# Performance work log

Measured on AMD Instinct MI355X. Metric: run time of the kernel, lower is better.

The kernel has to match this reference:

```python
import jax, jax.numpy as jnp
import numpy as np

# Sizes: B graphs of N nodes each, K nearest neighbours, D=feat_dim=nhid, C=pos_dim
B, N, K, D, C = 4, 1024, 128, 32, 2
L = 3                     # number of EGNN conv layers
E_IN = 2 * D + 1          # edge MLP input: feats_i | feats_j | rel_dist (edge_dim=0, fourier=0)
E_H = 2 * E_IN            # edge MLP hidden


def _lin(key, fan_in, fan_out):
    kw, kb = jax.random.split(key)
    w = jax.random.normal(kw, (fan_in, fan_out), jnp.float32) / np.sqrt(fan_in)
    b = jax.random.normal(kb, (fan_out,), jnp.float32) * 0.01
    return w, b


def _stack(key, fan_in, fan_out):
    ws, bs = zip(*[_lin(k, fan_in, fan_out) for k in jax.random.split(key, L)])
    return jnp.stack(ws), jnp.stack(bs)


def setup_inputs() -> dict:
    key = jax.random.key(0)
    ks = jax.random.split(key, 10)
    feat_ = jax.random.normal(ks[0], (B * N, D), jnp.float32)
    coor_ = jax.random.normal(ks[1], (B * N, C), jnp.float32)
    batch = jnp.full((B,), N, dtype=jnp.int32)   # per-graph node counts (equal-size graphs)
    embed_w, embed_b = _lin(ks[2], D, D)         # embed: Linear(feat_dim, nhid)
    e1_w, e1_b = _stack(ks[3], E_IN, E_H)        # edge MLP
    e2_w, e2_b = _stack(ks[4], E_H, D)           # -> m_dim = nhid
    gate_w, gate_b = _stack(ks[5], D, 1)         # soft_edges gate
    c1_w, c1_b = _stack(ks[6], D, 4 * D)         # coors MLP
    c2_w, c2_b = _stack(ks[7], 4 * D, 1)
    n1_w, n1_b = _stack(ks[8], 2 * D, 2 * D)     # node MLP
    n2_w, n2_b = _stack(ks[9], 2 * D, D)
    coors_scale = jnp.full((L, 1), 1e-2, jnp.float32)  # CoorsNorm scale (init 1e-2)
    return dict(feat_=feat_, coor_=coor_, batch=batch, embed_w=embed_w, embed_b=embed_b,
                e1_w=e1_w, e1_b=e1_b, e2_w=e2_w, e2_b=e2_b, gate_w=gate_w, gate_b=gate_b,
                c1_w=c1_w, c1_b=c1_b, c2_w=c2_w, c2_b=c2_b, n1_w=n1_w, n1_b=n1_b,
                n2_w=n2_w, n2_b=n2_b, coors_scale=coors_scale)


def _lrelu(x):
    return jax.nn.leaky_relu(x, 0.1)


def _gather(x, idx):
    # x: [B, n, d], idx: [B, n, k] -> [B, n, k, d]
    return jax.vmap(lambda xb, ib: xb[ib])(x, idx)


def _egnn_layer(feats, coors, p):
    (e1_w, e1_b, e2_w, e2_b, gate_w, gate_b, c1_w, c1_b, c2_w, c2_b,
     n1_w, n1_b, n2_w, n2_b, scale) = p
    # pairwise squared distances; k smallest (self included, valid_radius=inf)
    diff = coors[:, :, None, :] - coors[:, None, :, :]      # [B,n,n,C]
    dist = jnp.sum(diff * diff, axis=-1)                    # [B,n,n]
    neg_d, idx = jax.lax.top_k(-dist, K)                    # k nearest
    rel_dist = -neg_d[..., None]                            # [B,n,K,1]
    rel_coors = coors[:, :, None, :] - _gather(coors, idx)  # [B,n,K,C]
    feats_j = _gather(feats, idx)                           # [B,n,K,D]
    feats_i = jnp.broadcast_to(feats[:, :, None, :], feats_j.shape)
    edge_in = jnp.concatenate([feats_i, feats_j, rel_dist], axis=-1)  # [B,n,K,E_IN]
    # edge MLP: Lin -> act -> Lin -> act ; soft edge gate
    m = _lrelu(_lrelu(edge_in @ e1_w + e1_b) @ e2_w + e2_b)            # [B,n,K,D]
    m = m * jax.nn.sigmoid(m @ gate_w + gate_b)
    # coordinate update: coors_mlp -> scalar weights; CoorsNorm on rel coords
    cw = (_lrelu(m @ c1_w + c1_b) @ c2_w + c2_b)[..., 0]               # [B,n,K]
    norm = jnp.maximum(jnp.linalg.norm(rel_coors, axis=-1, keepdims=True), 1e-8)
    rel_n = rel_coors / norm * scale
    coors_out = jnp.einsum('bik,bikc->bic', cw, rel_n) + coors
    # feature update: sum-pool messages, node MLP with residual
    m_i = jnp.sum(m, axis=2)                                           # [B,n,D]
    node_in = jnp.concatenate([feats, m_i], axis=-1)
    feats_out = _lrelu(node_in @ n1_w + n1_b) @ n2_w + n2_b + feats
    return feats_out, coors_out


def reference(feat_, coor_, batch, embed_w, embed_b, e1_w, e1_b, e2_w, e2_b,
              gate_w, gate_b, c1_w, c1_b, c2_w, c2_b, n1_w, n1_b, n2_w, n2_b,
              coors_scale):
    # embed MLP (dropout is identity at p=0 / eval), then batch equal-size graphs
    feats = _lrelu(feat_ @ embed_w + embed_b).reshape(B, N, D)
    coors = coor_.reshape(B, N, C)
    for l in range(L):
        p = (e1_w[l], e1_b[l], e2_w[l], e2_b[l], gate_w[l], gate_b[l],
             c1_w[l], c1_b[l], c2_w[l], c2_b[l], n1_w[l], n1_b[l],
             n2_w[l], n2_b[l], coors_scale[l])
        feats, coors = _egnn_layer(feats, coors, p)
    return feats.reshape(B * N, D)
```

## Files before the change

### kernel.cpp

```cpp
#include <hip/hip_runtime.h>
#include <hip/hip_bf16.h>
#include <math.h>

#define BB 4
#define NN 1024
#define KK 128
#define DD 32
#define LL 3
#define EH 130
#define EHP 132

typedef float f32x4 __attribute__((ext_vector_type(4)));
typedef short s16x8 __attribute__((ext_vector_type(8)));

__device__ __forceinline__ float lrelu(float x) { return fmaxf(x, 0.1f * x); }

__device__ __forceinline__ unsigned pk2(float a, float b) {
    __hip_bfloat162 h = __float22bfloat162_rn(float2{a, b});
    return *(unsigned*)&h;
}
__device__ __forceinline__ unsigned short bf16_hu(float v) {
    return (unsigned short)((__float_as_uint(v) + 0x8000u) >> 16);
}
__device__ __forceinline__ unsigned short bf16_rne(float v) {
    unsigned u = __float_as_uint(v);
    return (unsigned short)((u + 0x7fffu + ((u >> 16) & 1u)) >> 16);
}

__device__ __forceinline__ void knn_block(const float2* __restrict__ cbp, int i, int t,
                                          unsigned* __restrict__ hist,
                                          volatile unsigned* __restrict__ scr,
                                          int* __restrict__ nb) {
    const int lane = t & 63, wid = t >> 6;
    unsigned* histw = hist + wid * 256;
    const float2 ci = cbp[i];
    unsigned k[4];
#pragma unroll
    for (int s = 0; s < 4; s++) {
        float2 cj = cbp[wid * 256 + s * 64 + lane];
        float dx = ci.x - cj.x, dy = ci.y - cj.y;
        float d = __fadd_rn(__fmul_rn(dx, dx), __fmul_rn(dy, dy));
        k[s] = __float_as_uint(d);
    }
    unsigned prefix = 0u;
    unsigned r = KK - 1;
#pragma unroll
    for (int pass = 0; pass < 4; pass++) {
        const int sh = 24 - 8 * pass;
        const unsigned mpref = (pass == 0) ? 0u : (0xFFFFFFFFu << (sh + 8));
        ((uint4*)histw)[lane] = uint4{0u, 0u, 0u, 0u};
#pragma unroll
        for (int s = 0; s < 4; s++) {
            if ((k[s] & mpref) == prefix)
                atomicAdd(&histw[(k[s] >> sh) & 255u], 1u);
        }
        __syncthreads();
        unsigned tot = hist[t] + hist[256 + t] + hist[512 + t] + hist[768 + t];
        unsigned incl = tot;
#pragma unroll
        for (int off = 1; off < 64; off <<= 1) {
            unsigned v = __shfl_up(incl, off, 64);
            if (lane >= off) incl += v;
        }
        if (lane == 63) scr[wid] = incl;
        __syncthreads();
        unsigned woff = 0;
#pragma unroll
        for (int w = 0; w < 4; w++)
            if (w < wid) woff += scr[w];
        incl += woff;
        const unsigned excl = incl - tot;
        if (r >= excl && r < incl) { scr[4] = (unsigned)t; scr[5] = r - excl; }
        __syncthreads();
        prefix |= scr[4] << sh;
        r = scr[5];
    }
    const unsigned dstar = prefix;

    const unsigned long long below = (1ull << lane) - 1ull;
    unsigned long long mL[4], mE[4];
    unsigned cntL = 0, cntE = 0;
#pragma unroll
    for (int s = 0; s < 4; s++) {
        mL[s] = __ballot(k[s] < dstar);
        mE[s] = __ballot(k[s] == dstar);
        cntL += (unsigned)__popcll(mL[s]);
        cntE += (unsigned)__popcll(mE[s]);
    }
    if (lane == 0) { scr[8 + wid] = cntL; scr[12 + wid] = cntE; }
    __syncthreads();
    unsigned offL = 0, offE = 0, totalL = 0;
#pragma unroll
    for (int w = 0; w < 4; w++) {
        unsigned cl = scr[8 + w];
        if (w < wid) { offL += cl; offE += scr[12 + w]; }
        totalL += cl;
    }
    unsigned run = offL;
#pragma unroll
    for (int s = 0; s < 4; s++) {
        if (k[s] < dstar) nb[run + (unsigned)__popcll(mL[s] & below)] = wid * 256 + s * 64 + lane;
        run += (unsigned)__popcll(mL[s]);
    }
    const int need = KK - (int)totalL;
    unsigned tie = offE;
#pragma unroll
    for (int s = 0; s < 4; s++) {
        if (k[s] == dstar) {
            unsigned r2 = tie + (unsigned)__popcll(mE[s] & below);
            if ((int)r2 < need) nb[totalL + r2] = wid * 256 + s * 64 + lane;
        }
        tie += (unsigned)__popcll(mE[s]);
    }
}

__global__ __launch_bounds__(128) void prep_kernel(
    const float* __restrict__ feat,
    const float* __restrict__ ew, const float* __restrict__ eb,
    float* __restrict__ fout,
    const float* __restrict__ e1w0, const float* __restrict__ e1b0,
    float* __restrict__ HI, float* __restrict__ HJ,
    const float* __restrict__ e2w, const float* __restrict__ e2b,
    const float* __restrict__ c1w,
    unsigned short* __restrict__ e2f, unsigned short* __restrict__ c1f) {
    const int bid = blockIdx.x;
    const int t = threadIdx.x;
    if (bid < 2048) {
        __shared__ float sfe[2][DD];
        const int n0 = bid * 2;
        if (t < 64) {
            const int nl = t >> 5, o = t & 31;
            const float* f = feat + (size_t)(n0 + nl) * DD;
            float a = eb[o];
#pragma unroll
            for (int k = 0; k < DD; k++) a = fmaf(f[k], ew[k * DD + o], a);
            a = lrelu(a);
            fout[(size_t)(n0 + nl) * DD + o] = a;
            sfe[nl][o] = a;
        }
        __syncthreads();
        for (int idx = t; idx < 2 * EHP; idx += 128) {
            const int nl = idx / EHP, o = idx - nl * EHP;
            const size_t off = (size_t)(n0 + nl) * EHP + o;
            if (o >= EH) { HI[off] = 0.f; HJ[off] = 0.f; continue; }
            const float* fl = sfe[nl];
            float aa = e1b0[o], cc = 0.f;
#pragma unroll
            for (int k = 0; k < DD; k++) aa = fmaf(fl[k], e1w0[k * EH + o], aa);
#pragma unroll
            for (int k = 0; k < DD; k++) cc = fmaf(fl[k], e1w0[(DD + k) * EH + o], cc);
            HI[off] = aa;
            HJ[off] = cc;
        }
    } else {
        const int TOT_E2 = LL * 5120;
        const int TOT = TOT_E2 + LL * 4096;
        for (int u = (bid - 2048) * 128 + t; u < TOT; u += 96 * 128) {
            if (u < TOT_E2) {
                int l = u / 5120, v = u - l * 5120;
                int jj = v & 7, la = (v >> 3) & 63, nt = (v >> 9) & 1, c = v >> 10;
                int n = nt * 16 + (la & 15);
                float val;
                if (c < 4) {
                    int k = 32 * c + (la >> 4) * 8 + jj;
                    val = e2w[(size_t)l * EH * DD + k * DD + n];
                } else {
                    int ks = (la >> 4) * 8 + jj;
                    val = (ks == 0) ? e2w[((size_t)l * EH + 128) * DD + n]
                        : (ks == 1) ? e2w[((size_t)l * EH + 129) * DD + n]
                        : (ks == 2) ? e2b[(size_t)l * DD + n] : 0.f;
                }
                e2f[u] = bf16_rne(val);
            } else {
                int v = u - TOT_E2;
                int jj = v & 7, la = (v >> 3) & 63, nt = (v >> 9) & 7, l = v >> 12;
                int k = (la >> 4) * 8 + jj;
                int n = nt * 16 + (la & 15);
                c1f[v] = bf16_rne(c1w[(size_t)l * DD * 128 + k * 128 + n]);
            }
        }
    }
}

__global__ __launch_bounds__(256) void layer_kernel(
    const float* __restrict__ feats_in, const float* __restrict__ coors_in,
    const float* __restrict__ HI, const float* __restrict__ HJ,
    const float* __restrict__ w65,
    const unsigned short* __restrict__ e2f,
    const unsigned short* __restrict__ c1f,
    const float* __restrict__ gw, const float* __restrict__ gb,
    const float* __restrict__ c1b, const float* __restrict__ c2w, const float* __restrict__ c2b,
    const float* __restrict__ n1w, const float* __restrict__ n1b,
    const float* __restrict__ n2w, const float* __restrict__ n2b,
    const float* __restrict__ scale,
    const float* __restrict__ e1wn, const float* __restrict__ e1bn,
    float* __restrict__ HIn, float* __restrict__ HJn,
    float* __restrict__ feats_out, float* __restrict__ coors_out) {
    const int node = blockIdx.x;
    const int b = node >> 10;
    const int t = threadIdx.x;
    const int lane = t & 63, wid = t >> 6;
    const int ln = lane & 15, q = lane >> 4;
    const int rowbase = wid * 32;

    __shared__ __align__(16) float shi[EHP];
    __shared__ __align__(16) float sw65[EHP];
    __shared__ __align__(16) unsigned short smA[4 * 32 * 32];
    __shared__ unsigned sknn[16];
    __shared__ float sx0[128], sx1[128], su[128], sv[128], srd[128];
    __shared__ int snb[128];
    __shared__ float sgw[DD], sfi[DD], sfo[DD];
    __shared__ float sc1b[128], sc2w[128];
    __shared__ float redm[4][DD], redc[4][2];
    __shared__ float sni[2 * DD], shd[2 * DD];
    __shared__ float sp1[4][2 * DD], sp2[4][DD];

    for (int u = t; u < EHP; u += 256) {
        shi[u] = HI[(size_t)node * EHP + u];
        sw65[u] = (u < EH) ? w65[u] : 0.f;
    }
    if (t < DD) { sfi[t] = feats_in[node * DD + t]; sgw[t] = gw[t]; }
    if (t >= 128) { sc1b[t - 128] = c1b[t - 128]; sc2w[t - 128] = c2w[t - 128]; }

    knn_block((const float2*)coors_in + (size_t)b * NN, node & (NN - 1), t,
              (unsigned*)smA, sknn, snb);
    __syncthreads();

    const float cix = coors_in[node * 2], ciy = coors_in[node * 2 + 1];
    if (t < 128) {
        const int j = snb[t];
        const float2 cj = *(const float2*)(coors_in + ((size_t)(b * NN) + j) * 2);
        const float dx = cix - cj.x, dy = ciy - cj.y;
        const float rd = __fadd_rn(__fmul_rn(dx, dx), __fmul_rn(dy, dy));
        srd[t] = rd;
        const float nrm = fmaxf(sqrtf(rd), 1e-8f);
        const float s = scale[0] / nrm;
        su[t] = dx * s;
        sv[t] = dy * s;
        const float2 hjt = *(const float2*)(HJ + ((size_t)(b * NN) + j) * EHP + 128);
        sx0[t] = lrelu(shi[128] + hjt.x + rd * sw65[128]);
        sx1[t] = lrelu(shi[129] + hjt.y + rd * sw65[129]);
    }
    __syncthreads();

    float rdR[2];
    const float* hjb[2];
#pragma unroll
    for (int mt = 0; mt < 2; mt++) {
        const int row = rowbase + mt * 16 + ln;
        rdR[mt] = srd[row];
        hjb[mt] = HJ + ((size_t)(b * NN) + snb[row]) * EHP;
    }

    const float4* shi4 = (const float4*)shi;
    const float4* sw4  = (const float4*)sw65;

    const f32x4 zz = {0.f, 0.f, 0.f, 0.f};
    f32x4 accA[2][2];
    accA[0][0] = zz; accA[0][1] = zz; accA[1][0] = zz; accA[1][1] = zz;

    float4 ha[2], hbv[2];
#pragma unroll
    for (int mt = 0; mt < 2; mt++) {
        const float4* hjp = (const float4*)(hjb[mt] + q * 8);
        ha[mt] = hjp[0];
        hbv[mt] = hjp[1];
    }
    s16x8 bcur0 = *(const s16x8*)(e2f + (0 * 64 + lane) * 8);
    s16x8 bcur1 = *(const s16x8*)(e2f + (1 * 64 + lane) * 8);

#pragma unroll 1
    for (int c = 0; c < 4; c++) {
        s16x8 bn0 = *(const s16x8*)(e2f + (((c + 1) * 2 + 0) * 64 + lane) * 8);
        s16x8 bn1 = *(const s16x8*)(e2f + (((c + 1) * 2 + 1) * 64 + lane) * 8);
        float4 nha[2], nhb[2];
        if (c < 3) {
#pragma unroll
            for (int mt = 0; mt < 2; mt++) {
                const float4* hjp = (const float4*)(hjb[mt] + (c + 1) * 32 + q * 8);
                nha[mt] = hjp[0];
                nhb[mt] = hjp[1];
            }
        }
        const int kb = c * 8 + q * 2;
        const float4 hi0 = shi4[kb], hi1 = shi4[kb + 1];
        const float4 wv0 = sw4[kb],  wv1 = sw4[kb + 1];
#pragma unroll
        for (int mt = 0; mt < 2; mt++) {
            const float r = rdR[mt];
            union { s16x8 v; unsigned u[4]; } A;
            A.u[0] = pk2(lrelu(hi0.x + ha[mt].x + r * wv0.x), lrelu(hi0.y + ha[mt].y + r * wv0.y));
            A.u[1] = pk2(lrelu(hi0.z + ha[mt].z + r * wv0.z), lrelu(hi0.w + ha[mt].w + r * wv0.w));
            A.u[2] = pk2(lrelu(hi1.x + hbv[mt].x + r * wv1.x), lrelu(hi1.y + hbv[mt].y + r * wv1.y));
            A.u[3] = pk2(lrelu(hi1.z + hbv[mt].z + r * wv1.z), lrelu(hi1.w + hbv[mt].w + r * wv1.w));
            accA[mt][0] = __builtin_amdgcn_mfma_f32_16x16x32_bf16(A.v, bcur0, accA[mt][0], 0, 0, 0);
            accA[mt][1] = __builtin_amdgcn_mfma_f32_16x16x32_bf16(A.v, bcur1, accA[mt][1], 0, 0, 0);
        }
#pragma unroll
        for (int mt = 0; mt < 2; mt++) { ha[mt] = nha[mt]; hbv[mt] = nhb[mt]; }
        bcur0 = bn0; bcur1 = bn1;
    }

    {
#pragma unroll
        for (int mt = 0; mt < 2; mt++) {
            const int row = rowbase + mt * 16 + ln;
            union { s16x8 v; unsigned u[4]; } A;
            const unsigned p0 = pk2(sx0[row], sx1[row]);
            A.u[0] = (q == 0) ? p0 : 0u;
            A.u[1] = (q == 0) ? 0x00003f80u : 0u;
            A.u[2] = 0u;
            A.u[3] = 0u;
            accA[mt][0] = __builtin_amdgcn_mfma_f32_16x16x32_bf16(A.v, bcur0, accA[mt][0], 0, 0, 0);
            accA[mt][1] = __builtin_amdgcn_mfma_f32_16x16x32_bf16(A.v, bcur1, accA[mt][1], 0, 0, 0);
        }
    }

    s16x8 cfr[8];
#pragma unroll
    for (int g8 = 0; g8 < 8; g8++)
        cfr[g8] = *(const s16x8*)(c1f + (g8 * 64 + lane) * 8);

#pragma unroll
    for (int mt = 0; mt < 2; mt++)
#pragma unroll
        for (int nt = 0; nt < 2; nt++)
#pragma unroll
            for (int r = 0; r < 4; r++)
                accA[mt][nt][r] = lrelu(accA[mt][nt][r]);

    const float gbv = gb[0];
#pragma unroll
    for (int mt = 0; mt < 2; mt++) {
        float p[4];
#pragma unroll
        for (int r = 0; r < 4; r++)
            p[r] = accA[mt][0][r] * sgw[ln] + accA[mt][1][r] * sgw[16 + ln];
#pragma unroll
        for (int off = 1; off <= 8; off <<= 1)
#pragma unroll
            for (int r = 0; r < 4; r++) p[r] += __shfl_xor(p[r], off);
#pragma unroll
        for (int r = 0; r < 4; r++) {
            const float g = 1.f / (1.f + __expf(-(p[r] + gbv)));
            accA[mt][0][r] *= g;
            accA[mt][1][r] *= g;
        }
    }

    float mi0 = 0.f, mi1 = 0.f;
#pragma unroll
    for (int mt = 0; mt < 2; mt++)
#pragma unroll
        for (int r = 0; r < 4; r++) { mi0 += accA[mt][0][r]; mi1 += accA[mt][1][r]; }
    mi0 += __shfl_xor(mi0, 16); mi0 += __shfl_xor(mi0, 32);
    mi1 += __shfl_xor(mi1, 16); mi1 += __shfl_xor(mi1, 32);
    if (lane < 16) { redm[wid][lane] = mi0; redm[wid][16 + lane] = mi1; }

    unsigned short* smw = smA + wid * (32 * 32);
#pragma unroll
    for (int mt = 0; mt < 2; mt++)
#pragma unroll
        for (int nt = 0; nt < 2; nt++)
#pragma unroll
            for (int r = 0; r < 4; r++) {
                const int prow = (r << 3) | (4 * mt + q);
                smw[prow * 32 + nt * 16 + ln] = bf16_hu(accA[mt][nt][r]);
            }

    s16x8 a4[2];
#pragma unroll
    for (int mt = 0; mt < 2; mt++) {
        const int prow = ((ln & 3) << 3) | (4 * mt + (ln >> 2));
        a4[mt] = *(const s16x8*)(smw + prow * 32 + q * 8);
    }

    float cacc[2][4];
#pragma unroll
    for (int mt = 0; mt < 2; mt++)
#pragma unroll
        for (int r = 0; r < 4; r++) cacc[mt][r] = 0.f;

#pragma unroll
    for (int g = 0; g < 4; g++) {
        const float cb0 = sc1b[(2 * g + 0) * 16 + ln];
        const float cb1 = sc1b[(2 * g + 1) * 16 + ln];
        const f32x4 ci0 = {cb0, cb0, cb0, cb0};
        const f32x4 ci1 = {cb1, cb1, cb1, cb1};
        f32x4 c20[2], c21[2];
#pragma unroll
        for (int mt = 0; mt < 2; mt++) {
            c20[mt] = __builtin_amdgcn_mfma_f32_16x16x32_bf16(a4[mt], cfr[2 * g + 0], ci0, 0, 0, 0);
            c21[mt] = __builtin_amdgcn_mfma_f32_16x16x32_bf16(a4[mt], cfr[2 * g + 1], ci1, 0, 0, 0);
        }
#pragma unroll
        for (int h = 0; h < 2; h++) {
            const float c2wv = sc2w[(2 * g + h) * 16 + ln];
#pragma unroll
            for (int mt = 0; mt < 2; mt++)
#pragma unroll
                for (int r = 0; r < 4; r++) {
                    const float v = (h ? c21[mt][r] : c20[mt][r]);
                    cacc[mt][r] = fmaf(lrelu(v), c2wv, cacc[mt][r]);
                }
        }
    }
#pragma unroll
    for (int off = 1; off <= 8; off <<= 1)
#pragma unroll
        for (int mt = 0; mt < 2; mt++)
#pragma unroll
            for (int r = 0; r < 4; r++) cacc[mt][r] += __shfl_xor(cacc[mt][r], off);

    const float c2bv = c2b[0];
    float vxp = 0.f, vyp = 0.f;
    if (ln == 0) {
#pragma unroll
        for (int mt = 0; mt < 2; mt++)
#pragma unroll
            for (int r = 0; r < 4; r++) {
                const int row = rowbase + mt * 16 + q * 4 + r;
                const float cw = cacc[mt][r] + c2bv;
                vxp = fmaf(cw, su[row], vxp);
                vyp = fmaf(cw, sv[row], vyp);
            }
    }
    vxp += __shfl_xor(vxp, 16); vxp += __shfl_xor(vxp, 32);
    vyp += __shfl_xor(vyp, 16); vyp += __shfl_xor(vyp, 32);
    if (lane == 0) { redc[wid][0] = vxp; redc[wid][1] = vyp; }

    __syncthreads();
    if (t < DD) {
        sni[t] = sfi[t];
        sni[DD + t] = redm[0][t] + redm[1][t] + redm[2][t] + redm[3][t];
    }
    __syncthreads();
    {
        const int o = t & 63, p = t >> 6;
        float a = 0.f;
#pragma unroll
        for (int k = 0; k < 16; k++) a = fmaf(sni[p * 16 + k], n1w[(p * 16 + k) * 64 + o], a);
        sp1[p][o] = a;
    }
    __syncthreads();
    if (t < 2 * DD)
        shd[t] = lrelu(n1b[t] + ((sp1[0][t] + sp1[1][t]) + (sp1[2][t] + sp1[3][t])));
    __syncthreads();
    if (t < 128) {
        const int o = t & 31, p = t >> 5;
        float a = 0.f;
#pragma unroll
        for (int k = 0; k < 16; k++) a = fmaf(shd[p * 16 + k], n2w[(p * 16 + k) * DD + o], a);
        sp2[p][o] = a;
    }
    __syncthreads();
    if (t < DD) {
        const float val = n2b[t] + ((sp2[0][t] + sp2[1][t]) + (sp2[2][t] + sp2[3][t])) + sfi[t];
        feats_out[node * DD + t] = val;
        sfo[t] = val;
    }
    if (t == 0) {
        coors_out[node * 2]     = cix + redc[0][0] + redc[1][0] + redc[2][0] + redc[3][0];
        coors_out[node * 2 + 1] = ciy + redc[0][1] + redc[1][1] + redc[2][1] + redc[3][1];
    }
    __syncthreads();

    if (e1wn) {
        for (int idx = t; idx < 2 * EHP; idx += 256) {
            const int nl = idx / EHP, o = idx - nl * EHP;
            float* dst = (nl ? HJn : HIn) + (size_t)node * EHP + o;
            if (o >= EH) { *dst = 0.f; continue; }
            const int rowoff = nl ? DD : 0;
            float a = nl ? 0.f : e1bn[o];
#pragma unroll
            for (int k = 0; k < DD; k++) a = fmaf(sfo[k], e1wn[(rowoff + k) * EH + o], a);
            *dst = a;
        }
    }
}

extern "C" void kernel_launch(void* const* d_in, const int* in_sizes, int n_in,
                              void* d_out, int out_size, void* d_ws, size_t ws_size,
                              hipStream_t stream) {
    const float* feat_   = (const float*)d_in[0];
    const float* coor_   = (const float*)d_in[1];
    const float* embed_w = (const float*)d_in[3];
    const float* embed_b = (const float*)d_in[4];
    const float* e1_w    = (const float*)d_in[5];
    const float* e1_b    = (const float*)d_in[6];
    const float* e2_w    = (const float*)d_in[7];
    const float* e2_b    = (const float*)d_in[8];
    const float* gate_w  = (const float*)d_in[9];
    const float* gate_b  = (const float*)d_in[10];
    const float* c1_w    = (const float*)d_in[11];
    const float* c1_b    = (const float*)d_in[12];
    const float* c2_w    = (const float*)d_in[13];
    const float* c2_b    = (const float*)d_in[14];
    const float* n1_w    = (const float*)d_in[15];
    const float* n1_b    = (const float*)d_in[16];
    const float* n2_w    = (const float*)d_in[17];
    const float* n2_b    = (const float*)d_in[18];
    const float* cscale  = (const float*)d_in[19];

    float* ws = (float*)d_ws;
    float* fa   = ws;   ws += BB * NN * DD;
    float* fb   = ws;   ws += BB * NN * DD;
    float* ca   = ws;   ws += BB * NN * 2;
    float* cb2  = ws;   ws += BB * NN * 2;
    float* HI0  = ws;   ws += BB * NN * EHP;
    float* HJ0  = ws;   ws += BB * NN * EHP;
    float* HI1  = ws;   ws += BB * NN * EHP;
    float* HJ1  = ws;   ws += BB * NN * EHP;
    unsigned short* e2f = (unsigned short*)ws;
    unsigned short* c1f = e2f + LL * 5120;

    prep_kernel<<<2048 + 96, 128, 0, stream>>>(feat_, embed_w, embed_b, fa,
                                               e1_w, e1_b, HI0, HJ0,
                                               e2_w, e2_b, c1_w, e2f, c1f);

    float* HIbuf[2] = {HI0, HI1};
    float* HJbuf[2] = {HJ0, HJ1};
    const float* fin = fa;
    const float* cin = coor_;
    float* fouts[LL] = {fb, fa, (float*)d_out};
    float* couts[LL] = {ca, cb2, ca};

    for (int l = 0; l < LL; l++) {
        const int cur = l & 1, nxt = (l + 1) & 1;
        layer_kernel<<<BB * NN, 256, 0, stream>>>(
            fin, cin, HIbuf[cur], HJbuf[cur],
            e1_w + ((size_t)l * 65 + 64) * EH,
            e2f + (size_t)l * 5120,
            c1f + (size_t)l * 4096,
            gate_w + (size_t)l * DD,
            gate_b + l,
            c1_b + (size_t)l * 128,
            c2_w + (size_t)l * 128,
            c2_b + l,
            n1_w + (size_t)l * 64 * 64,
            n1_b + (size_t)l * 64,
            n2_w + (size_t)l * 64 * 32,
            n2_b + (size_t)l * DD,
            cscale + l,
            (l < LL - 1) ? (e1_w + (size_t)(l + 1) * 65 * EH) : nullptr,
            (l < LL - 1) ? (e1_b + (size_t)(l + 1) * EH) : nullptr,
            HIbuf[nxt], HJbuf[nxt],
            fouts[l], couts[l]);
        fin = fouts[l];
        cin = couts[l];
    }
}
```

Measured before the change: 316.8 us.

## Compute neighbor edge-MLP first layer in-kernel via split-bf16 MFMA instead of gathering HJ

Stops precomputing the per-node HI/HJ projections (130 floats each) and no longer gathers 132-float HJ rows for every neighbor. Each block now gathers the neighbor's 32-dim features, stored as bf16 hi/lo pairs, and recomputes the j-side projection with three bf16 MFMAs per tile (hi*hi, hi*lo, lo*hi) to stay near fp32 accuracy. The i-side projection is computed once per block in fp32. This cuts global gather traffic about fourfold, at the cost of extra MFMA work, LDS staging of the hidden activations, and a new prepacked weight layout.

```diff
diff --git a/kernel.cpp b/kernel.cpp
--- a/kernel.cpp
+++ b/kernel.cpp
@@ -8,7 +8,6 @@
 #define DD 32
 #define LL 3
 #define EH 130
-#define EHP 132
 
 typedef float f32x4 __attribute__((ext_vector_type(4)));
 typedef short s16x8 __attribute__((ext_vector_type(8)));
@@ -25,6 +24,9 @@
 __device__ __forceinline__ unsigned short bf16_rne(float v) {
     unsigned u = __float_as_uint(v);
     return (unsigned short)((u + 0x7fffu + ((u >> 16) & 1u)) >> 16);
+}
+__device__ __forceinline__ float bf2f(unsigned short h) {
+    return __uint_as_float(((unsigned)h) << 16);
 }
 
 __device__ __forceinline__ void knn_block(const float2* __restrict__ cbp, int i, int t,
@@ -117,16 +119,15 @@
 __global__ __launch_bounds__(128) void prep_kernel(
     const float* __restrict__ feat,
     const float* __restrict__ ew, const float* __restrict__ eb,
-    float* __restrict__ fout,
-    const float* __restrict__ e1w0, const float* __restrict__ e1b0,
-    float* __restrict__ HI, float* __restrict__ HJ,
+    float* __restrict__ fout, unsigned short* __restrict__ fouth, unsigned short* __restrict__ foutl,
+    const float* __restrict__ e1w,
     const float* __restrict__ e2w, const float* __restrict__ e2b,
     const float* __restrict__ c1w,
-    unsigned short* __restrict__ e2f, unsigned short* __restrict__ c1f) {
+    unsigned short* __restrict__ e2f, unsigned short* __restrict__ c1f,
+    unsigned short* __restrict__ e1Jh, unsigned short* __restrict__ e1Jl) {
     const int bid = blockIdx.x;
     const int t = threadIdx.x;
     if (bid < 2048) {
-        __shared__ float sfe[2][DD];
         const int n0 = bid * 2;
         if (t < 64) {
             const int nl = t >> 5, o = t & 31;
@@ -135,28 +136,19 @@
 #pragma unroll
             for (int k = 0; k < DD; k++) a = fmaf(f[k], ew[k * DD + o], a);
             a = lrelu(a);
-            fout[(size_t)(n0 + nl) * DD + o] = a;
-            sfe[nl][o] = a;
-        }
-        __syncthreads();
-        for (int idx = t; idx < 2 * EHP; idx += 128) {
-            const int nl = idx / EHP, o = idx - nl * EHP;
-            const size_t off = (size_t)(n0 + nl) * EHP + o;
-            if (o >= EH) { HI[off] = 0.f; HJ[off] = 0.f; continue; }
-            const float* fl = sfe[nl];
-            float aa = e1b0[o], cc = 0.f;
-#pragma unroll
-            for (int k = 0; k < DD; k++) aa = fmaf(fl[k], e1w0[k * EH + o], aa);
-#pragma unroll
-            for (int k = 0; k < DD; k++) cc = fmaf(fl[k], e1w0[(DD + k) * EH + o], cc);
-            HI[off] = aa;
-            HJ[off] = cc;
+            const size_t off = (size_t)(n0 + nl) * DD + o;
+            fout[off] = a;
+            const unsigned short h = bf16_rne(a);
+            fouth[off] = h;
+            foutl[off] = bf16_rne(a - bf2f(h));
         }
     } else {
-        const int TOT_E2 = LL * 5120;
-        const int TOT = TOT_E2 + LL * 4096;
-        for (int u = (bid - 2048) * 128 + t; u < TOT; u += 96 * 128) {
-            if (u < TOT_E2) {
+        const int A_ = LL * 5120;
+        const int B_ = A_ + LL * 4096;
+        const int C_ = B_ + LL * 4608;
+        const int TOT = C_ + LL * 4608;
+        for (int u = (bid - 2048) * 128 + t; u < TOT; u += 432 * 128) {
+            if (u < A_) {
                 int l = u / 5120, v = u - l * 5120;
                 int jj = v & 7, la = (v >> 3) & 63, nt = (v >> 9) & 1, c = v >> 10;
                 int n = nt * 16 + (la & 15);
@@ -171,31 +163,46 @@
                         : (ks == 2) ? e2b[(size_t)l * DD + n] : 0.f;
                 }
                 e2f[u] = bf16_rne(val);
-            } else {
-                int v = u - TOT_E2;
+            } else if (u < B_) {
+                int v = u - A_;
                 int jj = v & 7, la = (v >> 3) & 63, nt = (v >> 9) & 7, l = v >> 12;
                 int k = (la >> 4) * 8 + jj;
                 int n = nt * 16 + (la & 15);
                 c1f[v] = bf16_rne(c1w[(size_t)l * DD * 128 + k * 128 + n]);
+            } else {
+                const int isLo = (u >= C_);
+                int v = u - (isLo ? C_ : B_);
+                int l = v / 4608, w = v - l * 4608;
+                int jj = w & 7, la = (w >> 3) & 63, nt = w >> 9;
+                int col = nt * 16 + (la & 15);
+                int k = (la >> 4) * 8 + jj;
+                float val = (col < EH) ? e1w[(size_t)l * 65 * EH + (size_t)(DD + k) * EH + col] : 0.f;
+                const unsigned short h = bf16_rne(val);
+                if (!isLo) e1Jh[v] = h;
+                else       e1Jl[v] = bf16_rne(val - bf2f(h));
             }
         }
     }
 }
 
 __global__ __launch_bounds__(256) void layer_kernel(
-    const float* __restrict__ feats_in, const float* __restrict__ coors_in,
-    const float* __restrict__ HI, const float* __restrict__ HJ,
+    const float* __restrict__ feats_in,
+    const unsigned short* __restrict__ finh, const unsigned short* __restrict__ finl,
+    const float* __restrict__ coors_in,
+    const float* __restrict__ e1wI,
+    const float* __restrict__ e1b_l,
     const float* __restrict__ w65,
     const unsigned short* __restrict__ e2f,
     const unsigned short* __restrict__ c1f,
+    const unsigned short* __restrict__ e1Jh, const unsigned short* __restrict__ e1Jl,
     const float* __restrict__ gw, const float* __restrict__ gb,
     const float* __restrict__ c1b, const float* __restrict__ c2w, const float* __restrict__ c2b,
     const float* __restrict__ n1w, const float* __restrict__ n1b,
     const float* __restrict__ n2w, const float* __restrict__ n2b,
     const float* __restrict__ scale,
-    const float* __restrict__ e1wn, const float* __restrict__ e1bn,
-    float* __restrict__ HIn, float* __restrict__ HJn,
-    float* __restrict__ feats_out, float* __restrict__ coors_out) {
+    float* __restrict__ feats_out,
+    unsigned short* __restrict__ fouth, unsigned short* __restrict__ foutl,
+    float* __restrict__ coors_out) {
     const int node = blockIdx.x;
     const int b = node >> 10;
     const int t = threadIdx.x;
@@ -203,24 +210,31 @@
     const int ln = lane & 15, q = lane >> 4;
     const int rowbase = wid * 32;
 
-    __shared__ __align__(16) float shi[EHP];
-    __shared__ __align__(16) float sw65[EHP];
+    __shared__ __align__(16) float shi[144];
+    __shared__ __align__(16) float sw65[144];
     __shared__ __align__(16) unsigned short smA[4 * 32 * 32];
     __shared__ unsigned sknn[16];
     __shared__ float sx0[128], sx1[128], su[128], sv[128], srd[128];
     __shared__ int snb[128];
-    __shared__ float sgw[DD], sfi[DD], sfo[DD];
+    __shared__ float sgw[DD], sfi[DD];
     __shared__ float sc1b[128], sc2w[128];
     __shared__ float redm[4][DD], redc[4][2];
     __shared__ float sni[2 * DD], shd[2 * DD];
     __shared__ float sp1[4][2 * DD], sp2[4][DD];
 
-    for (int u = t; u < EHP; u += 256) {
-        shi[u] = HI[(size_t)node * EHP + u];
-        sw65[u] = (u < EH) ? w65[u] : 0.f;
-    }
+    for (int u = t; u < 144; u += 256) sw65[u] = (u < EH) ? w65[u] : 0.f;
     if (t < DD) { sfi[t] = feats_in[node * DD + t]; sgw[t] = gw[t]; }
-    if (t >= 128) { sc1b[t - 128] = c1b[t - 128]; sc2w[t - 128] = c2w[t - 128]; }
+    if (t >= 128 && t < 256) { sc1b[t - 128] = c1b[t - 128]; sc2w[t - 128] = c2w[t - 128]; }
+    __syncthreads();
+
+    if (t < EH) {
+        float a = e1b_l[t];
+#pragma unroll
+        for (int k = 0; k < DD; k++) a = fmaf(sfi[k], e1wI[k * EH + t], a);
+        shi[t] = a;
+    } else if (t < 144) {
+        shi[t] = 0.f;
+    }
 
     knn_block((const float2*)coors_in + (size_t)b * NN, node & (NN - 1), t,
               (unsigned*)smA, sknn, snb);
@@ -237,71 +251,88 @@
         const float s = scale[0] / nrm;
         su[t] = dx * s;
         sv[t] = dy * s;
-        const float2 hjt = *(const float2*)(HJ + ((size_t)(b * NN) + j) * EHP + 128);
-        sx0[t] = lrelu(shi[128] + hjt.x + rd * sw65[128]);
-        sx1[t] = lrelu(shi[129] + hjt.y + rd * sw65[129]);
-    }
-    __syncthreads();
-
-    float rdR[2];
-    const float* hjb[2];
+    }
+    __syncthreads();
+
+    s16x8 ah[2], al[2];
+    float rd8[2][4];
 #pragma unroll
     for (int mt = 0; mt < 2; mt++) {
         const int row = rowbase + mt * 16 + ln;
-        rdR[mt] = srd[row];
-        hjb[mt] = HJ + ((size_t)(b * NN) + snb[row]) * EHP;
-    }
-
-    const float4* shi4 = (const float4*)shi;
-    const float4* sw4  = (const float4*)sw65;
+        const size_t jb = ((size_t)(b * NN) + snb[row]) * DD;
+        ah[mt] = *(const s16x8*)(finh + jb + q * 8);
+        al[mt] = *(const s16x8*)(finl + jb + q * 8);
+#pragma unroll
+        for (int r = 0; r < 4; r++) rd8[mt][r] = srd[rowbase + mt * 16 + q * 4 + r];
+    }
 
     const f32x4 zz = {0.f, 0.f, 0.f, 0.f};
     f32x4 accA[2][2];
     accA[0][0] = zz; accA[0][1] = zz; accA[1][0] = zz; accA[1][1] = zz;
-
-    float4 ha[2], hbv[2];
-#pragma unroll
-    for (int mt = 0; mt < 2; mt++) {
-        const float4* hjp = (const float4*)(hjb[mt] + q * 8);
-        ha[mt] = hjp[0];
-        hbv[mt] = hjp[1];
-    }
-    s16x8 bcur0 = *(const s16x8*)(e2f + (0 * 64 + lane) * 8);
-    s16x8 bcur1 = *(const s16x8*)(e2f + (1 * 64 + lane) * 8);
+    unsigned short* smw = smA + wid * (32 * 32);
 
 #pragma unroll 1
     for (int c = 0; c < 4; c++) {
-        s16x8 bn0 = *(const s16x8*)(e2f + (((c + 1) * 2 + 0) * 64 + lane) * 8);
-        s16x8 bn1 = *(const s16x8*)(e2f + (((c + 1) * 2 + 1) * 64 + lane) * 8);
-        float4 nha[2], nhb[2];
-        if (c < 3) {
-#pragma unroll
-            for (int mt = 0; mt < 2; mt++) {
-                const float4* hjp = (const float4*)(hjb[mt] + (c + 1) * 32 + q * 8);
-                nha[mt] = hjp[0];
-                nhb[mt] = hjp[1];
+        s16x8 bh0 = *(const s16x8*)(e1Jh + ((c * 2 + 0) * 64 + lane) * 8);
+        s16x8 bl0 = *(const s16x8*)(e1Jl + ((c * 2 + 0) * 64 + lane) * 8);
+        s16x8 bh1 = *(const s16x8*)(e1Jh + ((c * 2 + 1) * 64 + lane) * 8);
+        s16x8 bl1 = *(const s16x8*)(e1Jl + ((c * 2 + 1) * 64 + lane) * 8);
+        const float h0 = shi[c * 32 + ln],      h1 = shi[c * 32 + 16 + ln];
+        const float w0 = sw65[c * 32 + ln],     w1 = sw65[c * 32 + 16 + ln];
+        const f32x4 ci0 = {h0, h0, h0, h0};
+        const f32x4 ci1 = {h1, h1, h1, h1};
+#pragma unroll
+        for (int mt = 0; mt < 2; mt++) {
+            f32x4 s0 = __builtin_amdgcn_mfma_f32_16x16x32_bf16(ah[mt], bh0, ci0, 0, 0, 0);
+            s0 = __builtin_amdgcn_mfma_f32_16x16x32_bf16(ah[mt], bl0, s0, 0, 0, 0);
+            s0 = __builtin_amdgcn_mfma_f32_16x16x32_bf16(al[mt], bh0, s0, 0, 0, 0);
+            f32x4 s1 = __builtin_amdgcn_mfma_f32_16x16x32_bf16(ah[mt], bh1, ci1, 0, 0, 0);
+            s1 = __builtin_amdgcn_mfma_f32_16x16x32_bf16(ah[mt], bl1, s1, 0, 0, 0);
+            s1 = __builtin_amdgcn_mfma_f32_16x16x32_bf16(al[mt], bh1, s1, 0, 0, 0);
+#pragma unroll
+            for (int r = 0; r < 4; r++) {
+                const float x0 = lrelu(fmaf(rd8[mt][r], w0, s0[r]));
+                const float x1 = lrelu(fmaf(rd8[mt][r], w1, s1[r]));
+                const int prow = (r << 3) | (4 * mt + q);
+                smw[prow * 32 + ln] = bf16_hu(x0);
+                smw[prow * 32 + 16 + ln] = bf16_hu(x1);
             }
         }
-        const int kb = c * 8 + q * 2;
-        const float4 hi0 = shi4[kb], hi1 = shi4[kb + 1];
-        const float4 wv0 = sw4[kb],  wv1 = sw4[kb + 1];
+        s16x8 b0 = *(const s16x8*)(e2f + ((c * 2 + 0) * 64 + lane) * 8);
+        s16x8 b1 = *(const s16x8*)(e2f + ((c * 2 + 1) * 64 + lane) * 8);
 #pragma unroll
         for (int mt = 0; mt < 2; mt++) {
-            const float r = rdR[mt];
-            union { s16x8 v; unsigned u[4]; } A;
-            A.u[0] = pk2(lrelu(hi0.x + ha[mt].x + r * wv0.x), lrelu(hi0.y + ha[mt].y + r * wv0.y));
-            A.u[1] = pk2(lrelu(hi0.z + ha[mt].z + r * wv0.z), lrelu(hi0.w + ha[mt].w + r * wv0.w));
-            A.u[2] = pk2(lrelu(hi1.x + hbv[mt].x + r * wv1.x), lrelu(hi1.y + hbv[mt].y + r * wv1.y));
-            A.u[3] = pk2(lrelu(hi1.z + hbv[mt].z + r * wv1.z), lrelu(hi1.w + hbv[mt].w + r * wv1.w));
-            accA[mt][0] = __builtin_amdgcn_mfma_f32_16x16x32_bf16(A.v, bcur0, accA[mt][0], 0, 0, 0);
-            accA[mt][1] = __builtin_amdgcn_mfma_f32_16x16x32_bf16(A.v, bcur1, accA[mt][1], 0, 0, 0);
-        }
-#pragma unroll
-        for (int mt = 0; mt < 2; mt++) { ha[mt] = nha[mt]; hbv[mt] = nhb[mt]; }
-        bcur0 = bn0; bcur1 = bn1;
+            const int prow = ((ln & 3) << 3) | (4 * mt + (ln >> 2));
+            s16x8 a4x = *(const s16x8*)(smw + prow * 32 + q * 8);
+            accA[mt][0] = __builtin_amdgcn_mfma_f32_16x16x32_bf16(a4x, b0, accA[mt][0], 0, 0, 0);
+            accA[mt][1] = __builtin_amdgcn_mfma_f32_16x16x32_bf16(a4x, b1, accA[mt][1], 0, 0, 0);
+        }
     }
 
     {
+        s16x8 bh8 = *(const s16x8*)(e1Jh + (8 * 64 + lane) * 8);
+        s16x8 bl8 = *(const s16x8*)(e1Jl + (8 * 64 + lane) * 8);
+        const float h8 = shi[128 + ln];
+        const float w8 = sw65[128 + ln];
+        const f32x4 ci8 = {h8, h8, h8, h8};
+#pragma unroll
+        for (int mt = 0; mt < 2; mt++) {
+            f32x4 s = __builtin_amdgcn_mfma_f32_16x16x32_bf16(ah[mt], bh8, ci8, 0, 0, 0);
+            s = __builtin_amdgcn_mfma_f32_16x16x32_bf16(ah[mt], bl8, s, 0, 0, 0);
+            s = __builtin_amdgcn_mfma_f32_16x16x32_bf16(al[mt], bh8, s, 0, 0, 0);
+#pragma unroll
+            for (int r = 0; r < 4; r++) {
+                const float v = lrelu(fmaf(rd8[mt][r], w8, s[r]));
+                const int row = rowbase + mt * 16 + q * 4 + r;
+                if (ln == 0) sx0[row] = v;
+                else if (ln == 1) sx1[row] = v;
+            }
+        }
+    }
+
+    {
+        s16x8 b40 = *(const s16x8*)(e2f + (8 * 64 + lane) * 8);
+        s16x8 b41 = *(const s16x8*)(e2f + (9 * 64 + lane) * 8);
 #pragma unroll
         for (int mt = 0; mt < 2; mt++) {
             const int row = rowbase + mt * 16 + ln;
@@ -311,8 +342,8 @@
             A.u[1] = (q == 0) ? 0x00003f80u : 0u;
             A.u[2] = 0u;
             A.u[3] = 0u;
-            accA[mt][0] = __builtin_amdgcn_mfma_f32_16x16x32_bf16(A.v, bcur0, accA[mt][0], 0, 0, 0);
-            accA[mt][1] = __builtin_amdgcn_mfma_f32_16x16x32_bf16(A.v, bcur1, accA[mt][1], 0, 0, 0);
+            accA[mt][0] = __builtin_amdgcn_mfma_f32_16x16x32_bf16(A.v, b40, accA[mt][0], 0, 0, 0);
+            accA[mt][1] = __builtin_amdgcn_mfma_f32_16x16x32_bf16(A.v, b41, accA[mt][1], 0, 0, 0);
         }
     }
 
@@ -357,7 +388,6 @@
     mi1 += __shfl_xor(mi1, 16); mi1 += __shfl_xor(mi1, 32);
     if (lane < 16) { redm[wid][lane] = mi0; redm[wid][16 + lane] = mi1; }
 
-    unsigned short* smw = smA + wid * (32 * 32);
 #pragma unroll
     for (int mt = 0; mt < 2; mt++)
 #pragma unroll
@@ -457,25 +487,15 @@
     if (t < DD) {
         const float val = n2b[t] + ((sp2[0][t] + sp2[1][t]) + (sp2[2][t] + sp2[3][t])) + sfi[t];
         feats_out[node * DD + t] = val;
-        sfo[t] = val;
+        if (fouth) {
+            const unsigned short h = bf16_rne(val);
+            fouth[node * DD + t] = h;
+            foutl[node * DD + t] = bf16_rne(val - bf2f(h));
+        }
     }
     if (t == 0) {
         coors_out[node * 2]     = cix + redc[0][0] + redc[1][0] + redc[2][0] + redc[3][0];
         coors_out[node * 2 + 1] = ciy + redc[0][1] + redc[1][1] + redc[2][1] + redc[3][1];
-    }
-    __syncthreads();
-
-    if (e1wn) {
-        for (int idx = t; idx < 2 * EHP; idx += 256) {
-            const int nl = idx / EHP, o = idx - nl * EHP;
-            float* dst = (nl ? HJn : HIn) + (size_t)node * EHP + o;
-            if (o >= EH) { *dst = 0.f; continue; }
-            const int rowoff = nl ? DD : 0;
-            float a = nl ? 0.f : e1bn[o];
-#pragma unroll
-            for (int k = 0; k < DD; k++) a = fmaf(sfo[k], e1wn[(rowoff + k) * EH + o], a);
-            *dst = a;
-        }
     }
 }
 
@@ -507,31 +527,39 @@
     float* fb   = ws;   ws += BB * NN * DD;
     float* ca   = ws;   ws += BB * NN * 2;
     float* cb2  = ws;   ws += BB * NN * 2;
-    float* HI0  = ws;   ws += BB * NN * EHP;
-    float* HJ0  = ws;   ws += BB * NN * EHP;
-    float* HI1  = ws;   ws += BB * NN * EHP;
-    float* HJ1  = ws;   ws += BB * NN * EHP;
-    unsigned short* e2f = (unsigned short*)ws;
-    unsigned short* c1f = e2f + LL * 5120;
-
-    prep_kernel<<<2048 + 96, 128, 0, stream>>>(feat_, embed_w, embed_b, fa,
-                                               e1_w, e1_b, HI0, HJ0,
-                                               e2_w, e2_b, c1_w, e2f, c1f);
-
-    float* HIbuf[2] = {HI0, HI1};
-    float* HJbuf[2] = {HJ0, HJ1};
+    unsigned short* e2f  = (unsigned short*)ws;
+    unsigned short* c1f  = e2f + LL * 5120;
+    unsigned short* e1Jh = c1f + LL * 4096;
+    unsigned short* e1Jl = e1Jh + LL * 4608;
+    unsigned short* fah  = e1Jl + LL * 4608;
+    unsigned short* fal  = fah + BB * NN * DD;
+    unsigned short* fbh  = fal + BB * NN * DD;
+    unsigned short* fbl  = fbh + BB * NN * DD;
+
+    prep_kernel<<<2048 + 432, 128, 0, stream>>>(feat_, embed_w, embed_b,
+                                                fa, fah, fal,
+                                                e1_w, e2_w, e2_b, c1_w,
+                                                e2f, c1f, e1Jh, e1Jl);
+
     const float* fin = fa;
+    const unsigned short* finh = fah;
+    const unsigned short* finl = fal;
     const float* cin = coor_;
-    float* fouts[LL] = {fb, fa, (float*)d_out};
+    float* fouts[LL]          = {fb, fa, (float*)d_out};
+    unsigned short* fouth[LL] = {fbh, fah, nullptr};
+    unsigned short* foutl[LL] = {fbl, fal, nullptr};
     float* couts[LL] = {ca, cb2, ca};
 
     for (int l = 0; l < LL; l++) {
-        const int cur = l & 1, nxt = (l + 1) & 1;
         layer_kernel<<<BB * NN, 256, 0, stream>>>(
-            fin, cin, HIbuf[cur], HJbuf[cur],
+            fin, finh, finl, cin,
+            e1_w + (size_t)l * 65 * EH,
+            e1_b + (size_t)l * EH,
             e1_w + ((size_t)l * 65 + 64) * EH,
             e2f + (size_t)l * 5120,
             c1f + (size_t)l * 4096,
+            e1Jh + (size_t)l * 4608,
+            e1Jl + (size_t)l * 4608,
             gate_w + (size_t)l * DD,
             gate_b + l,
             c1_b + (size_t)l * 128,
@@ -542,11 +570,11 @@
             n2_w + (size_t)l * 64 * 32,
             n2_b + (size_t)l * DD,
             cscale + l,
-            (l < LL - 1) ? (e1_w + (size_t)(l + 1) * 65 * EH) : nullptr,
-            (l < LL - 1) ? (e1_b + (size_t)(l + 1) * EH) : nullptr,
-            HIbuf[nxt], HJbuf[nxt],
-            fouts[l], couts[l]);
+            fouts[l], fouth[l], foutl[l],
+            couts[l]);
         fin = fouts[l];
+        finh = fouth[l];
+        finl = foutl[l];
         cin = couts[l];
     }
 }
```

After: 322.4 us. No clear change (+1.8%).
